# Kernel tuning notes

Measured on AMD Instinct MI355X. Metric: run time of the kernel, lower is better.

The kernel has to match this reference:

```python
import jax, jax.numpy as jnp
import numpy as np

B, TQ, TM, D, ATTN, H = 8, 1024, 1024, 512, 512, 8
HEAD_DIM = ATTN // H
TEMPERATURE = 1.0
CAUSALITY = True
NEG_INF = -2.0 ** 32 + 1


def setup_inputs() -> dict:
    key = jax.random.key(0)
    ks = jax.random.split(key, 7)
    scale = 1.0 / np.sqrt(D)
    return {
        "inputs": jax.random.normal(ks[0], (B, TQ, D), dtype=jnp.float32),
        "memory": jax.random.normal(ks[1], (B, TM, D), dtype=jnp.float32),
        "Wq": jax.random.normal(ks[2], (D, ATTN), dtype=jnp.float32) * scale,
        "Wk": jax.random.normal(ks[3], (D, ATTN), dtype=jnp.float32) * scale,
        "Wv": jax.random.normal(ks[4], (D, ATTN), dtype=jnp.float32) * scale,
        "memory_lengths": jax.random.randint(ks[5], (B,), TM // 2, TM + 1, dtype=jnp.int32),
        "query_lengths": jax.random.randint(ks[6], (B,), TQ // 2, TQ + 1, dtype=jnp.int32),
    }


def _split_head(x):
    # [B, T, ATTN] -> [B, H, T, HEAD_DIM]
    b, t, _ = x.shape
    return x.reshape(b, t, H, HEAD_DIM).transpose(0, 2, 1, 3)


def reference(inputs, memory, Wq, Wk, Wv, memory_lengths, query_lengths):
    q = _split_head(inputs @ Wq)   # [B,H,Tq,hd]
    k = _split_head(memory @ Wk)   # [B,H,Tm,hd]
    v = _split_head(memory @ Wv)   # [B,H,Tm,hd]

    logits = jnp.einsum("bhqd,bhmd->bhqm", q, k)
    logits = logits / jnp.sqrt(jnp.float32(HEAD_DIM)) / TEMPERATURE

    mem_mask = jnp.arange(TM)[None, :] < memory_lengths[:, None]   # [B,Tm]
    qry_mask = jnp.arange(TQ)[None, :] < query_lengths[:, None]    # [B,Tq]
    length_mask = qry_mask[:, :, None] & mem_mask[:, None, :]      # [B,Tq,Tm]
    mask = length_mask[:, None, :, :]                              # [B,1,Tq,Tm]
    if CAUSALITY:
        causal = jnp.tril(jnp.ones((TQ, TM), dtype=bool))
        mask = mask & causal[None, None, :, :]

    logits = jnp.where(mask, logits, jnp.float32(NEG_INF))
    alignments = jax.nn.softmax(logits, axis=3)                    # [B,H,Tq,Tm]
    contexts = jnp.einsum("bhqm,bhmd->bhqd", alignments, v)
    contexts = contexts.transpose(0, 2, 1, 3).reshape(inputs.shape[0], TQ, ATTN)
    return contexts, alignments
```

## Files before the change

### kernel.cpp

```cpp
#include <hip/hip_runtime.h>

#define NB 8
#define NTQ 1024
#define NTM 1024
#define ND 512
#define NATTN 512
#define NH 8
#define NDH 64

typedef _Float16 half8 __attribute__((ext_vector_type(8)));
typedef float f32x4 __attribute__((ext_vector_type(4)));

__global__ __launch_bounds__(256) void wprep_kernel(
    const float* __restrict__ Wq, const float* __restrict__ Wk,
    const float* __restrict__ Wv, _Float16* __restrict__ Wt) {
  const int z = blockIdx.z;
  const float* __restrict__ W = (z == 0) ? Wq : ((z == 1) ? Wk : Wv);
  _Float16* __restrict__ out = Wt + (size_t)z * NATTN * ND;
  const int k0 = blockIdx.x * 64;
  const int n0 = blockIdx.y * 64;
  __shared__ __align__(16) _Float16 Ls[64][72];
  const int t = threadIdx.x;
  const int sr = t >> 2, sc = (t & 3) * 16;
  const float4* src = (const float4*)(W + (size_t)(k0 + sr) * NATTN + n0 + sc);
  float4 f0 = src[0], f1 = src[1], f2 = src[2], f3 = src[3];
  float gv[16];
  *(float4*)&gv[0] = f0; *(float4*)&gv[4] = f1;
  *(float4*)&gv[8] = f2; *(float4*)&gv[12] = f3;
#pragma unroll
  for (int j = 0; j < 16; j++) Ls[sc + j][sr] = (_Float16)gv[j];
  __syncthreads();
  _Float16* dst = out + (size_t)(n0 + sr) * ND + k0 + sc;
  *(half8*)dst = *(const half8*)&Ls[sr][sc];
  *(half8*)(dst + 8) = *(const half8*)&Ls[sr][sc + 8];
}

__global__ __launch_bounds__(256) void proj_kernel(
    const float* __restrict__ inputs, const float* __restrict__ memory,
    const _Float16* __restrict__ Wt, _Float16* __restrict__ Qh,
    _Float16* __restrict__ Kh, _Float16* __restrict__ Vth) {
  const int id = blockIdx.x;
  const int xcd = id & 7;
  const int g = id >> 3;
  const int z = g >> 6;
  const int gg = g & 63;
  const int row0 = (xcd * 16 + (gg >> 2)) * 64;
  const int col0 = (gg & 3) * 128;

  const float* __restrict__ A = (z == 0) ? inputs : memory;
  const _Float16* __restrict__ Wz = Wt + (size_t)z * NATTN * ND;

  __shared__ __align__(16) _Float16 pool[64 * 72 + 128 * 72];
  _Float16* Asb = pool;
  _Float16* Wsb = pool + 64 * 72;

  const int t = threadIdx.x;
  const int w = t >> 6, L = t & 63;
  const int lrow = L & 15, quad = L >> 4;
  const int sr = t >> 2, sc = (t & 3) * 16;
  const int sr2 = t >> 1, sc2 = (t & 1) * 32;

  const f32x4 zf = {0.f, 0.f, 0.f, 0.f};
  f32x4 acc[8];
#pragma unroll
  for (int i = 0; i < 8; i++) acc[i] = zf;

  for (int k0 = 0; k0 < ND; k0 += 64) {
    {
      const float4* src = (const float4*)(A + (size_t)(row0 + sr) * ND + k0 + sc);
      float4 f0 = src[0], f1 = src[1], f2 = src[2], f3 = src[3];
      half8 h0, h1;
      h0[0] = (_Float16)f0.x; h0[1] = (_Float16)f0.y; h0[2] = (_Float16)f0.z; h0[3] = (_Float16)f0.w;
      h0[4] = (_Float16)f1.x; h0[5] = (_Float16)f1.y; h0[6] = (_Float16)f1.z; h0[7] = (_Float16)f1.w;
      h1[0] = (_Float16)f2.x; h1[1] = (_Float16)f2.y; h1[2] = (_Float16)f2.z; h1[3] = (_Float16)f2.w;
      h1[4] = (_Float16)f3.x; h1[5] = (_Float16)f3.y; h1[6] = (_Float16)f3.z; h1[7] = (_Float16)f3.w;
      *(half8*)&Asb[sr * 72 + sc] = h0;
      *(half8*)&Asb[sr * 72 + sc + 8] = h1;
    }
    {
      const half8* wsrc = (const half8*)(Wz + (size_t)(col0 + sr2) * ND + k0 + sc2);
#pragma unroll
      for (int j = 0; j < 4; j++) *(half8*)&Wsb[sr2 * 72 + sc2 + 8 * j] = wsrc[j];
    }
    __syncthreads();
#pragma unroll
    for (int ks = 0; ks < 2; ks++) {
      half8 a = *(const half8*)&Asb[(w * 16 + lrow) * 72 + ks * 32 + quad * 8];
#pragma unroll
      for (int nt = 0; nt < 8; nt++) {
        half8 b = *(const half8*)&Wsb[(nt * 16 + lrow) * 72 + ks * 32 + quad * 8];
        acc[nt] = __builtin_amdgcn_mfma_f32_16x16x32_f16(a, b, acc[nt], 0, 0, 0);
      }
    }
    __syncthreads();
  }

  const int bb = row0 >> 10;
  const int tr0 = row0 & 1023;
  const int hh0 = col0 >> 6;

  if (z <= 1) {
#pragma unroll
    for (int nt = 0; nt < 8; nt++)
#pragma unroll
      for (int r = 0; r < 4; r++)
        pool[(w * 16 + quad * 4 + r) * 136 + nt * 16 + lrow] = (_Float16)acc[nt][r];
    __syncthreads();
    const int sce = (t & 3) * 32;
    _Float16* base = (z == 0) ? Qh : Kh;
    _Float16* dst = base + (size_t)(bb * NH + hh0 + (sce >> 6)) * NTQ * NDH +
                    (size_t)(tr0 + sr) * NDH + (sce & 63);
#pragma unroll
    for (int j = 0; j < 4; j++)
      *(half8*)(dst + 8 * j) = *(const half8*)&pool[sr * 136 + sce + 8 * j];
  } else {
#pragma unroll
    for (int nt = 0; nt < 8; nt++)
#pragma unroll
      for (int r = 0; r < 4; r++)
        Wsb[(nt * 16 + lrow) * 72 + w * 16 + quad * 4 + r] = (_Float16)acc[nt][r];
    __syncthreads();
    _Float16* dst = Vth +
        ((size_t)(bb * NH + hh0 + (sr2 >> 6)) * NDH + (sr2 & 63)) * NTM + tr0 + sc2;
#pragma unroll
    for (int j = 0; j < 4; j++)
      *(half8*)(dst + 8 * j) = *(const half8*)&Wsb[sr2 * 72 + sc2 + 8 * j];
  }
}

__global__ __launch_bounds__(256) void attn_kernel(
    const _Float16* __restrict__ Qh, const _Float16* __restrict__ Kh,
    const _Float16* __restrict__ Vth, const int* __restrict__ mem_len,
    const int* __restrict__ qry_len, float* __restrict__ ctx_out,
    float* __restrict__ align_out) {
  const int bh = blockIdx.x;
  const int qt = blockIdx.y;
  const int bb = bh >> 3;
  const int hh = bh & 7;
  const int q0 = qt * 64;

  __shared__ __align__(16) _Float16 Qs[64][72];
  __shared__ __align__(16) _Float16 Ks[64][72];
  __shared__ __align__(16) _Float16 Vts[64][72];
  __shared__ __align__(16) _Float16 Ps[4][16][72];

  const int t = threadIdx.x, w = t >> 6, L = t & 63;
  const int lrow = L & 15, quad = L >> 4;
  const int qlen = qry_len[bb], mlen = mem_len[bb];
  const int mtop = (mlen + 63) >> 6;
  const int n_comp = (q0 + 63 >= qlen) ? 16 : min(qt + 1, mtop);
  const _Float16* Qbase = Qh + (size_t)bh * NTQ * NDH;
  const _Float16* Kbase = Kh + (size_t)bh * NTM * NDH;
  const _Float16* Vbase = Vth + (size_t)bh * NDH * NTM;
  const int sr = t >> 2, sc = (t & 3) * 16;
  const f32x4 zf = {0.f, 0.f, 0.f, 0.f};
  float* abase = align_out + (size_t)bh * NTQ * NTM;

  if (n_comp < 16) {
    const int c0 = n_comp * 64;
    float* rp = abase + (size_t)(q0 + sr) * NTM;
    const float4 z4 = {0.f, 0.f, 0.f, 0.f};
    for (int c = c0 + (t & 3) * 4; c < NTM; c += 16) *(float4*)(rp + c) = z4;
  }

  {
    const half8* src = (const half8*)(Qbase + (size_t)(q0 + sr) * NDH + sc);
    *(half8*)&Qs[sr][sc] = src[0];
    *(half8*)&Qs[sr][sc + 8] = src[1];
  }
  const int qg = q0 + w * 16 + quad * 4;
  float rowsum[4] = {0.f, 0.f, 0.f, 0.f};
  __syncthreads();

  for (int mt = 0; mt < n_comp; mt++) {
    {
      const half8* src = (const half8*)(Kbase + (size_t)(mt * 64 + sr) * NDH + sc);
      *(half8*)&Ks[sr][sc] = src[0];
      *(half8*)&Ks[sr][sc + 8] = src[1];
    }
    __syncthreads();
    f32x4 sacc[4];
#pragma unroll
    for (int i = 0; i < 4; i++) sacc[i] = zf;
#pragma unroll
    for (int ks = 0; ks < 2; ks++) {
      half8 a = *(const half8*)&Qs[w * 16 + lrow][ks * 32 + quad * 8];
#pragma unroll
      for (int nt = 0; nt < 4; nt++) {
        half8 b = *(const half8*)&Ks[nt * 16 + lrow][ks * 32 + quad * 8];
        sacc[nt] = __builtin_amdgcn_mfma_f32_16x16x32_f16(a, b, sacc[nt], 0, 0, 0);
      }
    }
#pragma unroll
    for (int nt = 0; nt < 4; nt++) {
      int m = mt * 64 + nt * 16 + lrow;
#pragma unroll
      for (int r = 0; r < 4; r++) {
        int q = qg + r;
        float p;
        if (q >= qlen) p = 1.0f;
        else if (m > q || m >= mlen) p = 0.0f;
        else p = __expf(sacc[nt][r] * 0.125f);
        rowsum[r] += p;
      }
    }
    __syncthreads();
  }
  float inv[4];
#pragma unroll
  for (int r = 0; r < 4; r++) {
    float s = rowsum[r];
    s += __shfl_xor(s, 1, 16);
    s += __shfl_xor(s, 2, 16);
    s += __shfl_xor(s, 4, 16);
    s += __shfl_xor(s, 8, 16);
    inv[r] = 1.0f / s;
  }

  f32x4 cacc[4];
#pragma unroll
  for (int i = 0; i < 4; i++) cacc[i] = zf;

  for (int mt = 0; mt < n_comp; mt++) {
    {
      const half8* src = (const half8*)(Kbase + (size_t)(mt * 64 + sr) * NDH + sc);
      *(half8*)&Ks[sr][sc] = src[0];
      *(half8*)&Ks[sr][sc + 8] = src[1];
      const half8* vsrc = (const half8*)(Vbase + (size_t)sr * NTM + mt * 64 + sc);
      *(half8*)&Vts[sr][sc] = vsrc[0];
      *(half8*)&Vts[sr][sc + 8] = vsrc[1];
    }
    __syncthreads();
    f32x4 sacc[4];
#pragma unroll
    for (int i = 0; i < 4; i++) sacc[i] = zf;
#pragma unroll
    for (int ks = 0; ks < 2; ks++) {
      half8 a = *(const half8*)&Qs[w * 16 + lrow][ks * 32 + quad * 8];
#pragma unroll
      for (int nt = 0; nt < 4; nt++) {
        half8 b = *(const half8*)&Ks[nt * 16 + lrow][ks * 32 + quad * 8];
        sacc[nt] = __builtin_amdgcn_mfma_f32_16x16x32_f16(a, b, sacc[nt], 0, 0, 0);
      }
    }
#pragma unroll
    for (int nt = 0; nt < 4; nt++) {
      int m = mt * 64 + nt * 16 + lrow;
#pragma unroll
      for (int r = 0; r < 4; r++) {
        int q = qg + r;
        float p;
        if (q >= qlen) p = inv[r];
        else if (m > q || m >= mlen) p = 0.0f;
        else p = __expf(sacc[nt][r] * 0.125f) * inv[r];
        abase[(size_t)q * NTM + m] = p;
        Ps[w][quad * 4 + r][nt * 16 + lrow] = (_Float16)p;
      }
    }
#pragma unroll
    for (int ks = 0; ks < 2; ks++) {
      half8 a = *(const half8*)&Ps[w][lrow][ks * 32 + quad * 8];
#pragma unroll
      for (int dt = 0; dt < 4; dt++) {
        half8 b = *(const half8*)&Vts[dt * 16 + lrow][ks * 32 + quad * 8];
        cacc[dt] = __builtin_amdgcn_mfma_f32_16x16x32_f16(a, b, cacc[dt], 0, 0, 0);
      }
    }
    __syncthreads();
  }

  float* cbase = ctx_out + (size_t)bb * NTQ * NATTN + (size_t)hh * NDH;
#pragma unroll
  for (int dt = 0; dt < 4; dt++) {
#pragma unroll
    for (int r = 0; r < 4; r++) {
      int q = qg + r;
      cbase[(size_t)q * NATTN + dt * 16 + lrow] = cacc[dt][r];
    }
  }
}

extern "C" void kernel_launch(void* const* d_in, const int* in_sizes, int n_in,
                              void* d_out, int out_size, void* d_ws,
                              size_t ws_size, hipStream_t stream) {
  const float* inputs = (const float*)d_in[0];
  const float* memory = (const float*)d_in[1];
  const float* Wq = (const float*)d_in[2];
  const float* Wk = (const float*)d_in[3];
  const float* Wv = (const float*)d_in[4];
  const int* mlen = (const int*)d_in[5];
  const int* qlen = (const int*)d_in[6];

  float* ctx = (float*)d_out;
  float* align = ctx + (size_t)NB * NTQ * NATTN;

  _Float16* Qh = (_Float16*)d_ws;
  _Float16* Kh = Qh + (size_t)NB * NH * NTQ * NDH;
  _Float16* Vth = Kh + (size_t)NB * NH * NTM * NDH;
  _Float16* Wt = (_Float16*)align;

  wprep_kernel<<<dim3(8, 8, 3), 256, 0, stream>>>(Wq, Wk, Wv, Wt);
  proj_kernel<<<dim3(1536), 256, 0, stream>>>(inputs, memory, Wt, Qh, Kh, Vth);
  attn_kernel<<<dim3(64, 16), 256, 0, stream>>>(Qh, Kh, Vth, mlen, qlen, ctx,
                                                align);
}
```

Before: 393.0 us.

## Handle fully-masked query rows with closed-form uniform softmax instead of full tile compute

Query rows beyond qlen have a uniform softmax over all 1024 keys. Previously any tile containing such rows swept all 16 key tiles through both passes. Now the causal path loops only up to min(qt+1, mtop) tiles and skips stores for rows past qlen. Padded rows instead get a closed-form result: the context is the mean of V, computed by a per-block reduction, and the alignments are filled with 1/1024 using vector stores. This removes most MFMA and exp work for tiles at or past qlen, at the cost of a redundant V-sum reduction in every such block.

```diff
diff --git a/kernel.cpp b/kernel.cpp
--- a/kernel.cpp
+++ b/kernel.cpp
@@ -143,139 +143,173 @@
   __shared__ __align__(16) _Float16 Ks[64][72];
   __shared__ __align__(16) _Float16 Vts[64][72];
   __shared__ __align__(16) _Float16 Ps[4][16][72];
+  __shared__ float vsum_lds[64];
 
   const int t = threadIdx.x, w = t >> 6, L = t & 63;
   const int lrow = L & 15, quad = L >> 4;
   const int qlen = qry_len[bb], mlen = mem_len[bb];
   const int mtop = (mlen + 63) >> 6;
-  const int n_comp = (q0 + 63 >= qlen) ? 16 : min(qt + 1, mtop);
+  const bool has_causal = q0 < qlen;
+  const bool has_uniform = (q0 + 64) > qlen;
+  const int n_comp = has_causal ? min(qt + 1, mtop) : 0;
   const _Float16* Qbase = Qh + (size_t)bh * NTQ * NDH;
   const _Float16* Kbase = Kh + (size_t)bh * NTM * NDH;
   const _Float16* Vbase = Vth + (size_t)bh * NDH * NTM;
   const int sr = t >> 2, sc = (t & 3) * 16;
   const f32x4 zf = {0.f, 0.f, 0.f, 0.f};
   float* abase = align_out + (size_t)bh * NTQ * NTM;
-
-  if (n_comp < 16) {
-    const int c0 = n_comp * 64;
-    float* rp = abase + (size_t)(q0 + sr) * NTM;
-    const float4 z4 = {0.f, 0.f, 0.f, 0.f};
-    for (int c = c0 + (t & 3) * 4; c < NTM; c += 16) *(float4*)(rp + c) = z4;
-  }
-
-  {
-    const half8* src = (const half8*)(Qbase + (size_t)(q0 + sr) * NDH + sc);
-    *(half8*)&Qs[sr][sc] = src[0];
-    *(half8*)&Qs[sr][sc + 8] = src[1];
-  }
-  const int qg = q0 + w * 16 + quad * 4;
-  float rowsum[4] = {0.f, 0.f, 0.f, 0.f};
-  __syncthreads();
-
-  for (int mt = 0; mt < n_comp; mt++) {
+  float* cbase = ctx_out + (size_t)bb * NTQ * NATTN + (size_t)hh * NDH;
+
+  if (has_causal) {
+    if (n_comp < 16) {
+      const int c0 = n_comp * 64;
+      const int row = q0 + sr;
+      if (row < qlen) {
+        float* rp = abase + (size_t)row * NTM;
+        const float4 z4 = {0.f, 0.f, 0.f, 0.f};
+        for (int c = c0 + (t & 3) * 4; c < NTM; c += 16) *(float4*)(rp + c) = z4;
+      }
+    }
     {
-      const half8* src = (const half8*)(Kbase + (size_t)(mt * 64 + sr) * NDH + sc);
-      *(half8*)&Ks[sr][sc] = src[0];
-      *(half8*)&Ks[sr][sc + 8] = src[1];
-    }
-    __syncthreads();
-    f32x4 sacc[4];
-#pragma unroll
-    for (int i = 0; i < 4; i++) sacc[i] = zf;
-#pragma unroll
-    for (int ks = 0; ks < 2; ks++) {
-      half8 a = *(const half8*)&Qs[w * 16 + lrow][ks * 32 + quad * 8];
+      const half8* src = (const half8*)(Qbase + (size_t)(q0 + sr) * NDH + sc);
+      *(half8*)&Qs[sr][sc] = src[0];
+      *(half8*)&Qs[sr][sc + 8] = src[1];
+    }
+    const int qg = q0 + w * 16 + quad * 4;
+    float rowsum[4] = {0.f, 0.f, 0.f, 0.f};
+    __syncthreads();
+
+    for (int mt = 0; mt < n_comp; mt++) {
+      {
+        const half8* src = (const half8*)(Kbase + (size_t)(mt * 64 + sr) * NDH + sc);
+        *(half8*)&Ks[sr][sc] = src[0];
+        *(half8*)&Ks[sr][sc + 8] = src[1];
+      }
+      __syncthreads();
+      f32x4 sacc[4];
+#pragma unroll
+      for (int i = 0; i < 4; i++) sacc[i] = zf;
+#pragma unroll
+      for (int ks = 0; ks < 2; ks++) {
+        half8 a = *(const half8*)&Qs[w * 16 + lrow][ks * 32 + quad * 8];
+#pragma unroll
+        for (int nt = 0; nt < 4; nt++) {
+          half8 b = *(const half8*)&Ks[nt * 16 + lrow][ks * 32 + quad * 8];
+          sacc[nt] = __builtin_amdgcn_mfma_f32_16x16x32_f16(a, b, sacc[nt], 0, 0, 0);
+        }
+      }
 #pragma unroll
       for (int nt = 0; nt < 4; nt++) {
-        half8 b = *(const half8*)&Ks[nt * 16 + lrow][ks * 32 + quad * 8];
-        sacc[nt] = __builtin_amdgcn_mfma_f32_16x16x32_f16(a, b, sacc[nt], 0, 0, 0);
-      }
-    }
-#pragma unroll
-    for (int nt = 0; nt < 4; nt++) {
-      int m = mt * 64 + nt * 16 + lrow;
+        int m = mt * 64 + nt * 16 + lrow;
+#pragma unroll
+        for (int r = 0; r < 4; r++) {
+          int q = qg + r;
+          float p;
+          if (q >= qlen) p = 0.0f;
+          else if (m > q || m >= mlen) p = 0.0f;
+          else p = __expf(sacc[nt][r] * 0.125f);
+          rowsum[r] += p;
+        }
+      }
+      __syncthreads();
+    }
+    float inv[4];
+#pragma unroll
+    for (int r = 0; r < 4; r++) {
+      float s = rowsum[r];
+      s += __shfl_xor(s, 1, 16);
+      s += __shfl_xor(s, 2, 16);
+      s += __shfl_xor(s, 4, 16);
+      s += __shfl_xor(s, 8, 16);
+      inv[r] = 1.0f / s;
+    }
+
+    f32x4 cacc[4];
+#pragma unroll
+    for (int i = 0; i < 4; i++) cacc[i] = zf;
+
+    for (int mt = 0; mt < n_comp; mt++) {
+      {
+        const half8* src = (const half8*)(Kbase + (size_t)(mt * 64 + sr) * NDH + sc);
+        *(half8*)&Ks[sr][sc] = src[0];
+        *(half8*)&Ks[sr][sc + 8] = src[1];
+        const half8* vsrc = (const half8*)(Vbase + (size_t)sr * NTM + mt * 64 + sc);
+        *(half8*)&Vts[sr][sc] = vsrc[0];
+        *(half8*)&Vts[sr][sc + 8] = vsrc[1];
+      }
+      __syncthreads();
+      f32x4 sacc[4];
+#pragma unroll
+      for (int i = 0; i < 4; i++) sacc[i] = zf;
+#pragma unroll
+      for (int ks = 0; ks < 2; ks++) {
+        half8 a = *(const half8*)&Qs[w * 16 + lrow][ks * 32 + quad * 8];
+#pragma unroll
+        for (int nt = 0; nt < 4; nt++) {
+          half8 b = *(const half8*)&Ks[nt * 16 + lrow][ks * 32 + quad * 8];
+          sacc[nt] = __builtin_amdgcn_mfma_f32_16x16x32_f16(a, b, sacc[nt], 0, 0, 0);
+        }
+      }
+#pragma unroll
+      for (int nt = 0; nt < 4; nt++) {
+        int m = mt * 64 + nt * 16 + lrow;
+#pragma unroll
+        for (int r = 0; r < 4; r++) {
+          int q = qg + r;
+          float p;
+          if (q >= qlen) p = 0.0f;
+          else if (m > q || m >= mlen) p = 0.0f;
+          else p = __expf(sacc[nt][r] * 0.125f) * inv[r];
+          if (q < qlen) abase[(size_t)q * NTM + m] = p;
+          Ps[w][quad * 4 + r][nt * 16 + lrow] = (_Float16)p;
+        }
+      }
+#pragma unroll
+      for (int ks = 0; ks < 2; ks++) {
+        half8 a = *(const half8*)&Ps[w][lrow][ks * 32 + quad * 8];
+#pragma unroll
+        for (int dt = 0; dt < 4; dt++) {
+          half8 b = *(const half8*)&Vts[dt * 16 + lrow][ks * 32 + quad * 8];
+          cacc[dt] = __builtin_amdgcn_mfma_f32_16x16x32_f16(a, b, cacc[dt], 0, 0, 0);
+        }
+      }
+      __syncthreads();
+    }
+
+#pragma unroll
+    for (int dt = 0; dt < 4; dt++) {
 #pragma unroll
       for (int r = 0; r < 4; r++) {
         int q = qg + r;
-        float p;
-        if (q >= qlen) p = 1.0f;
-        else if (m > q || m >= mlen) p = 0.0f;
-        else p = __expf(sacc[nt][r] * 0.125f);
-        rowsum[r] += p;
-      }
-    }
-    __syncthreads();
+        if (q < qlen) cbase[(size_t)q * NATTN + dt * 16 + lrow] = cacc[dt][r];
+      }
+    }
   }
-  float inv[4];
-#pragma unroll
-  for (int r = 0; r < 4; r++) {
-    float s = rowsum[r];
-    s += __shfl_xor(s, 1, 16);
-    s += __shfl_xor(s, 2, 16);
-    s += __shfl_xor(s, 4, 16);
-    s += __shfl_xor(s, 8, 16);
-    inv[r] = 1.0f / s;
-  }
-
-  f32x4 cacc[4];
-#pragma unroll
-  for (int i = 0; i < 4; i++) cacc[i] = zf;
-
-  for (int mt = 0; mt < n_comp; mt++) {
-    {
-      const half8* src = (const half8*)(Kbase + (size_t)(mt * 64 + sr) * NDH + sc);
-      *(half8*)&Ks[sr][sc] = src[0];
-      *(half8*)&Ks[sr][sc + 8] = src[1];
-      const half8* vsrc = (const half8*)(Vbase + (size_t)sr * NTM + mt * 64 + sc);
-      *(half8*)&Vts[sr][sc] = vsrc[0];
-      *(half8*)&Vts[sr][sc + 8] = vsrc[1];
-    }
-    __syncthreads();
-    f32x4 sacc[4];
-#pragma unroll
-    for (int i = 0; i < 4; i++) sacc[i] = zf;
-#pragma unroll
-    for (int ks = 0; ks < 2; ks++) {
-      half8 a = *(const half8*)&Qs[w * 16 + lrow][ks * 32 + quad * 8];
-#pragma unroll
-      for (int nt = 0; nt < 4; nt++) {
-        half8 b = *(const half8*)&Ks[nt * 16 + lrow][ks * 32 + quad * 8];
-        sacc[nt] = __builtin_amdgcn_mfma_f32_16x16x32_f16(a, b, sacc[nt], 0, 0, 0);
-      }
-    }
-#pragma unroll
-    for (int nt = 0; nt < 4; nt++) {
-      int m = mt * 64 + nt * 16 + lrow;
-#pragma unroll
-      for (int r = 0; r < 4; r++) {
-        int q = qg + r;
-        float p;
-        if (q >= qlen) p = inv[r];
-        else if (m > q || m >= mlen) p = 0.0f;
-        else p = __expf(sacc[nt][r] * 0.125f) * inv[r];
-        abase[(size_t)q * NTM + m] = p;
-        Ps[w][quad * 4 + r][nt * 16 + lrow] = (_Float16)p;
-      }
-    }
-#pragma unroll
-    for (int ks = 0; ks < 2; ks++) {
-      half8 a = *(const half8*)&Ps[w][lrow][ks * 32 + quad * 8];
-#pragma unroll
-      for (int dt = 0; dt < 4; dt++) {
-        half8 b = *(const half8*)&Vts[dt * 16 + lrow][ks * 32 + quad * 8];
-        cacc[dt] = __builtin_amdgcn_mfma_f32_16x16x32_f16(a, b, cacc[dt], 0, 0, 0);
-      }
-    }
-    __syncthreads();
-  }
-
-  float* cbase = ctx_out + (size_t)bb * NTQ * NATTN + (size_t)hh * NDH;
-#pragma unroll
-  for (int dt = 0; dt < 4; dt++) {
-#pragma unroll
-    for (int r = 0; r < 4; r++) {
-      int q = qg + r;
-      cbase[(size_t)q * NATTN + dt * 16 + lrow] = cacc[dt][r];
+
+  if (has_uniform) {
+    const int d = t >> 2;
+    const int seg = t & 3;
+    const _Float16* vp = Vbase + (size_t)d * NTM + seg * 256;
+    float s = 0.f;
+#pragma unroll
+    for (int j = 0; j < 32; j++) {
+      half8 v = *(const half8*)(vp + 8 * j);
+#pragma unroll
+      for (int e = 0; e < 8; e++) s += (float)v[e];
+    }
+    s += __shfl_xor(s, 1, 4);
+    s += __shfl_xor(s, 2, 4);
+    if (seg == 0) vsum_lds[d] = s * (1.0f / 1024.0f);
+    __syncthreads();
+    const int qu0 = (q0 > qlen) ? q0 : qlen;
+    for (int q = qu0 + w; q < q0 + 64; q += 4)
+      cbase[(size_t)q * NATTN + L] = vsum_lds[L];
+    const float cval = 1.0f / 1024.0f;
+    const f32x4 c4 = {cval, cval, cval, cval};
+    for (int q = qu0 + w; q < q0 + 64; q += 4) {
+      float* rp = abase + (size_t)q * NTM + L * 4;
+#pragma unroll
+      for (int j = 0; j < 4; j++) *(f32x4*)(rp + j * 256) = c4;
     }
   }
 }
```

Measured after the change: 384.2 us. 1.02x faster.
